# Optimization experiments

Hardware: AMD Instinct MI355X
Metric: run time of the kernel (lower is better)

## Reference

```python
import jax, jax.numpy as jnp
import numpy as np

DIST_THRESHOLD = 2.0
CONF_SIGMA = 1.0


def setup_inputs() -> dict:
    key = jax.random.key(0)
    k1, k2 = jax.random.split(key)
    pred_points = jax.random.normal(k1, (1024, 20, 2), dtype=jnp.float32)
    gt_points = jax.random.normal(k2, (2048, 20, 2), dtype=jnp.float32)
    return {"pred_points": pred_points, "gt_points": gt_points}


def reference(pred_points, gt_points):
    # pred_points: (N, P, 2), gt_points: (M, P, 2)
    # simple distance: mean over P of per-point Euclidean distance -> (N, M)
    diff = pred_points[:, None, :, :] - gt_points[None, :, :, :]  # (N, M, P, 2)
    distances = jnp.sqrt(jnp.sum(diff * diff, axis=-1)).mean(axis=-1)  # (N, M)
    min_distances = distances.min(axis=1)          # (N,)
    matched_indices = distances.argmin(axis=1)     # (N,) int
    matched_points = gt_points[matched_indices]    # (N, P, 2)
    confidence = jnp.where(
        min_distances > DIST_THRESHOLD,
        jnp.float32(0.0),
        jnp.exp(-min_distances / CONF_SIGMA),
    )[:, None]                                     # (N, 1)
    return matched_points, confidence, matched_indices
```

## Files before the change

kernel.cpp:

```cpp
#include <hip/hip_runtime.h>

#define N 1024
#define M 2048
#define P 20
#define THREADS 256
#define WAVES 4
#define CHUNKS 128
#define GROUPS 16
#define RPC (M / CHUNKS)
#define RPW (RPC / WAVES)
#define PSTRIDE 41

typedef unsigned long long u64;


__global__ __launch_bounds__(THREADS) void pm_partial(
    const float* __restrict__ pred, const float* __restrict__ gt,
    u64* __restrict__ best)
{
    const int tid   = threadIdx.x;
    const int wave  = tid >> 6;
    const int lane  = tid & 63;
    const int chunk = blockIdx.x;
    const int group = blockIdx.y;

    __shared__ float s_pred[64 * PSTRIDE];
    {
        const float4* psrc = (const float4*)(pred + group * 64 * 40);
        for (int t = tid; t < 64 * 10; t += THREADS) {
            float4 v = psrc[t];
            const int r = t / 10, j = t - r * 10;
            float* dst = &s_pred[r * PSTRIDE + 4 * j];
            dst[0] = v.x; dst[1] = v.y; dst[2] = v.z; dst[3] = v.w;
        }
    }
    __syncthreads();

    float pr[40];
#pragma unroll
    for (int e = 0; e < 40; ++e) pr[e] = s_pred[lane * PSTRIDE + e];

    float bd = 3.4e38f;
    int   bi = 0x7fffffff;
    const int m0 = chunk * RPC + wave * RPW;
#pragma unroll 2
    for (int r = 0; r < RPW; ++r) {
        const int m_u = __builtin_amdgcn_readfirstlane(m0 + r);
        const float4* gp = (const float4*)(gt + m_u * 40);
        float acc = 0.0f;
#pragma unroll
        for (int q = 0; q < 10; ++q) {
            float4 g = gp[q];
            float dx0 = pr[4*q+0] - g.x;
            float dy0 = pr[4*q+1] - g.y;
            float dx1 = pr[4*q+2] - g.z;
            float dy1 = pr[4*q+3] - g.w;
            acc += __builtin_amdgcn_sqrtf(dx0*dx0 + dy0*dy0);
            acc += __builtin_amdgcn_sqrtf(dx1*dx1 + dy1*dy1);
        }
        float dist = acc * (1.0f / P);
        if (dist < bd) { bd = dist; bi = m_u; }
    }

    u64 key = ((u64)__float_as_uint(bd) << 32) | (unsigned)bi;

    __shared__ u64 s_k[WAVES][64];
    s_k[wave][lane] = key;
    __syncthreads();
    if (wave == 0) {
        u64 k = s_k[0][lane];
#pragma unroll
        for (int w = 1; w < WAVES; ++w) {
            u64 o = s_k[w][lane];
            if (o < k) k = o;
        }
        atomicMin(&best[group * 64 + lane], k);
    }
}

__global__ __launch_bounds__(256) void pm_final(
    const float* __restrict__ gt, const u64* __restrict__ best,
    float* __restrict__ out)
{
    const int tid = threadIdx.x;
    const int blk = blockIdx.x;
    __shared__ int s_fi[64];

    if (tid < 64) {
        const int n = blk * 64 + tid;
        u64 k = best[n];
        float fd = __uint_as_float((unsigned)(k >> 32));
        int   fi = (int)(unsigned)(k & 0xffffffffu);
        out[40960 + n] = (fd > 2.0f) ? 0.0f : expf(-fd);
        out[41984 + n] = (float)fi;
        s_fi[tid] = fi;
    }
    __syncthreads();

    const int base_row = blk * 64;
    for (int t = tid; t < 64 * 40; t += 256) {
        const int r = t / 40;
        const int e = t - r * 40;
        out[(base_row + r) * 40 + e] = gt[s_fi[r] * 40 + e];
    }
}

extern "C" void kernel_launch(void* const* d_in, const int* in_sizes, int n_in,
                              void* d_out, int out_size, void* d_ws, size_t ws_size,
                              hipStream_t stream) {
    const float* pred = (const float*)d_in[0];
    const float* gt   = (const float*)d_in[1];
    float* out = (float*)d_out;
    u64*  best = (u64*)d_ws;
    (void)in_sizes; (void)n_in; (void)out_size; (void)ws_size;

    dim3 grid1(CHUNKS, GROUPS);
    pm_partial<<<grid1, THREADS, 0, stream>>>(pred, gt, best);
    pm_final<<<N / 64, 256, 0, stream>>>(gt, best, out);
}
```

Measured before the change: 70.54 us.

## Fuse distance argmin and gather into one kernel with per-lane gt rows

Replaces the two-kernel scheme (partial argmin with 64-bit atomicMin into workspace, then a finalize/gather kernel) with a single fused kernel. Each block now owns two prediction rows held in registers. Each thread scans a strided set of gt rows with per-lane vector loads, and the block reduces with wave shuffles and LDS before writing confidence, index and gathered points directly. This removes the second launch, the atomics and the workspace round-trip. In exchange it uses only 512 blocks of 256 threads, which gives low occupancy, and every block re-reads all of gt from cache with uncoalesced strided per-lane loads instead of scalar broadcasts.

Measured after the change: 65.21 us (median of 2 runs). 7.6% less time.

```diff
diff --git a/kernel.cpp b/kernel.cpp
--- a/kernel.cpp
+++ b/kernel.cpp
@@ -5,103 +5,107 @@
 #define P 20
 #define THREADS 256
 #define WAVES 4
-#define CHUNKS 128
-#define GROUPS 16
-#define RPC (M / CHUNKS)
-#define RPW (RPC / WAVES)
-#define PSTRIDE 41
+#define PPB 2
+#define BLOCKS (N / PPB)
+#define RPT (M / THREADS)
 
 typedef unsigned long long u64;
 
 
-__global__ __launch_bounds__(THREADS) void pm_partial(
+__device__ __forceinline__ u64 wave_min_u64(u64 k) {
+#pragma unroll
+    for (int off = 32; off > 0; off >>= 1) {
+        u64 o = __shfl_down(k, off, 64);
+        if (o < k) k = o;
+    }
+    return k;
+}
+
+__global__ __launch_bounds__(THREADS) void pm_fused(
     const float* __restrict__ pred, const float* __restrict__ gt,
-    u64* __restrict__ best)
+    float* __restrict__ out)
 {
-    const int tid   = threadIdx.x;
-    const int wave  = tid >> 6;
-    const int lane  = tid & 63;
-    const int chunk = blockIdx.x;
-    const int group = blockIdx.y;
+    const int tid  = threadIdx.x;
+    const int wave = tid >> 6;
+    const int lane = tid & 63;
+    const int n0   = blockIdx.x * PPB;
 
-    __shared__ float s_pred[64 * PSTRIDE];
+    float pr0[40], pr1[40];
     {
-        const float4* psrc = (const float4*)(pred + group * 64 * 40);
-        for (int t = tid; t < 64 * 10; t += THREADS) {
-            float4 v = psrc[t];
-            const int r = t / 10, j = t - r * 10;
-            float* dst = &s_pred[r * PSTRIDE + 4 * j];
-            dst[0] = v.x; dst[1] = v.y; dst[2] = v.z; dst[3] = v.w;
+        const float4* p0 = (const float4*)(pred + (n0 + 0) * 40);
+        const float4* p1 = (const float4*)(pred + (n0 + 1) * 40);
+#pragma unroll
+        for (int q = 0; q < 10; ++q) {
+            float4 a = p0[q];
+            pr0[4*q+0] = a.x; pr0[4*q+1] = a.y; pr0[4*q+2] = a.z; pr0[4*q+3] = a.w;
+            float4 b = p1[q];
+            pr1[4*q+0] = b.x; pr1[4*q+1] = b.y; pr1[4*q+2] = b.z; pr1[4*q+3] = b.w;
         }
+    }
+
+    float bd0 = 3.4e38f, bd1 = 3.4e38f;
+    int   bi0 = 0x7fffffff, bi1 = 0x7fffffff;
+    for (int i = 0; i < RPT; ++i) {
+        const int m = i * THREADS + tid;
+        const float4* gp = (const float4*)(gt + m * 40);
+        float acc0 = 0.0f, acc1 = 0.0f;
+#pragma unroll
+        for (int q = 0; q < 10; ++q) {
+            float4 g = gp[q];
+            float adx0 = pr0[4*q+0] - g.x;
+            float ady0 = pr0[4*q+1] - g.y;
+            float adx1 = pr0[4*q+2] - g.z;
+            float ady1 = pr0[4*q+3] - g.w;
+            acc0 += __builtin_amdgcn_sqrtf(adx0*adx0 + ady0*ady0);
+            acc0 += __builtin_amdgcn_sqrtf(adx1*adx1 + ady1*ady1);
+            float bdx0 = pr1[4*q+0] - g.x;
+            float bdy0 = pr1[4*q+1] - g.y;
+            float bdx1 = pr1[4*q+2] - g.z;
+            float bdy1 = pr1[4*q+3] - g.w;
+            acc1 += __builtin_amdgcn_sqrtf(bdx0*bdx0 + bdy0*bdy0);
+            acc1 += __builtin_amdgcn_sqrtf(bdx1*bdx1 + bdy1*bdy1);
+        }
+        float d0 = acc0 * (1.0f / P);
+        float d1 = acc1 * (1.0f / P);
+        if (d0 < bd0) { bd0 = d0; bi0 = m; }
+        if (d1 < bd1) { bd1 = d1; bi1 = m; }
+    }
+
+    u64 k0 = ((u64)__float_as_uint(bd0) << 32) | (unsigned)bi0;
+    u64 k1 = ((u64)__float_as_uint(bd1) << 32) | (unsigned)bi1;
+
+    k0 = wave_min_u64(k0);
+    k1 = wave_min_u64(k1);
+
+    __shared__ u64 s_k[2][WAVES];
+    __shared__ int s_fi[2];
+    if (lane == 0) { s_k[0][wave] = k0; s_k[1][wave] = k1; }
+    __syncthreads();
+
+    if (tid == 0) {
+        u64 b0 = s_k[0][0], b1 = s_k[1][0];
+#pragma unroll
+        for (int w = 1; w < WAVES; ++w) {
+            if (s_k[0][w] < b0) b0 = s_k[0][w];
+            if (s_k[1][w] < b1) b1 = s_k[1][w];
+        }
+        float fd0 = __uint_as_float((unsigned)(b0 >> 32));
+        float fd1 = __uint_as_float((unsigned)(b1 >> 32));
+        int   fi0 = (int)(unsigned)(b0 & 0xffffffffu);
+        int   fi1 = (int)(unsigned)(b1 & 0xffffffffu);
+        out[40960 + n0 + 0] = (fd0 > 2.0f) ? 0.0f : expf(-fd0);
+        out[40960 + n0 + 1] = (fd1 > 2.0f) ? 0.0f : expf(-fd1);
+        out[41984 + n0 + 0] = (float)fi0;
+        out[41984 + n0 + 1] = (float)fi1;
+        s_fi[0] = fi0;
+        s_fi[1] = fi1;
     }
     __syncthreads();
 
-    float pr[40];
-#pragma unroll
-    for (int e = 0; e < 40; ++e) pr[e] = s_pred[lane * PSTRIDE + e];
-
-    float bd = 3.4e38f;
-    int   bi = 0x7fffffff;
-    const int m0 = chunk * RPC + wave * RPW;
-#pragma unroll 2
-    for (int r = 0; r < RPW; ++r) {
-        const int m_u = __builtin_amdgcn_readfirstlane(m0 + r);
-        const float4* gp = (const float4*)(gt + m_u * 40);
-        float acc = 0.0f;
-#pragma unroll
-        for (int q = 0; q < 10; ++q) {
-            float4 g = gp[q];
-            float dx0 = pr[4*q+0] - g.x;
-            float dy0 = pr[4*q+1] - g.y;
-            float dx1 = pr[4*q+2] - g.z;
-            float dy1 = pr[4*q+3] - g.w;
-            acc += __builtin_amdgcn_sqrtf(dx0*dx0 + dy0*dy0);
-            acc += __builtin_amdgcn_sqrtf(dx1*dx1 + dy1*dy1);
-        }
-        float dist = acc * (1.0f / P);
-        if (dist < bd) { bd = dist; bi = m_u; }
-    }
-
-    u64 key = ((u64)__float_as_uint(bd) << 32) | (unsigned)bi;
-
-    __shared__ u64 s_k[WAVES][64];
-    s_k[wave][lane] = key;
-    __syncthreads();
-    if (wave == 0) {
-        u64 k = s_k[0][lane];
-#pragma unroll
-        for (int w = 1; w < WAVES; ++w) {
-            u64 o = s_k[w][lane];
-            if (o < k) k = o;
-        }
-        atomicMin(&best[group * 64 + lane], k);
-    }
-}
-
-__global__ __launch_bounds__(256) void pm_final(
-    const float* __restrict__ gt, const u64* __restrict__ best,
-    float* __restrict__ out)
-{
-    const int tid = threadIdx.x;
-    const int blk = blockIdx.x;
-    __shared__ int s_fi[64];
-
-    if (tid < 64) {
-        const int n = blk * 64 + tid;
-        u64 k = best[n];
-        float fd = __uint_as_float((unsigned)(k >> 32));
-        int   fi = (int)(unsigned)(k & 0xffffffffu);
-        out[40960 + n] = (fd > 2.0f) ? 0.0f : expf(-fd);
-        out[41984 + n] = (float)fi;
-        s_fi[tid] = fi;
-    }
-    __syncthreads();
-
-    const int base_row = blk * 64;
-    for (int t = tid; t < 64 * 40; t += 256) {
-        const int r = t / 40;
+    for (int t = tid; t < PPB * 40; t += THREADS) {
+        const int r = (t >= 40) ? 1 : 0;
         const int e = t - r * 40;
-        out[(base_row + r) * 40 + e] = gt[s_fi[r] * 40 + e];
+        out[(n0 + r) * 40 + e] = gt[s_fi[r] * 40 + e];
     }
 }
 
@@ -111,10 +115,7 @@
     const float* pred = (const float*)d_in[0];
     const float* gt   = (const float*)d_in[1];
     float* out = (float*)d_out;
-    u64*  best = (u64*)d_ws;
-    (void)in_sizes; (void)n_in; (void)out_size; (void)ws_size;
+    (void)in_sizes; (void)n_in; (void)out_size; (void)d_ws; (void)ws_size;
 
-    dim3 grid1(CHUNKS, GROUPS);
-    pm_partial<<<grid1, THREADS, 0, stream>>>(pred, gt, best);
-    pm_final<<<N / 64, 256, 0, stream>>>(gt, best, out);
+    pm_fused<<<dim3(BLOCKS), dim3(THREADS), 0, stream>>>(pred, gt, out);
 }
```
